# Performance work log

Hardware: AMD Instinct MI355X
Metric: run time of the kernel (lower is better)

The kernel has to match this reference:

```python
import jax, jax.numpy as jnp
import numpy as np
import math

B, NOUT, NCLASSES, CENTER, TOPK = 1024, 512, 5994, 3, 5
M, SUB_M, SCALE = 0.2, -0.06, 30.0

COS_M, SIN_M = math.cos(M), math.sin(M)
TH, MM = math.cos(math.pi - M), math.sin(math.pi - M) * M
SUB_COS_M, SUB_SIN_M = math.cos(SUB_M), math.sin(SUB_M)
SUB_TH, SUB_MM = math.cos(math.pi - SUB_M), math.sin(math.pi - SUB_M) * SUB_M


def setup_inputs() -> dict:
    key = jax.random.key(0)
    k1, k2, k3 = jax.random.split(key, 3)
    x = jax.random.normal(k1, (B, NOUT), dtype=jnp.float32)
    # xavier_normal over (center, nClasses, nOut): fan_in=nClasses*nOut, fan_out=center*nOut
    std = math.sqrt(2.0 / (NCLASSES * NOUT + CENTER * NOUT))
    weight = jax.random.normal(k2, (CENTER, NCLASSES, NOUT), dtype=jnp.float32) * std
    label = jax.random.randint(k3, (B,), 0, NCLASSES, dtype=jnp.int64)
    return {"x": x, "weight": weight, "label": label}


def _l2norm(v, axis=-1, eps=1e-12):
    return v / jnp.maximum(jnp.linalg.norm(v, axis=axis, keepdims=True), eps)


def reference(x, weight, label):
    xn = _l2norm(x)                       # [B, j]
    wn = _l2norm(weight)                  # [a, c, j]
    cosine_subcen = jnp.einsum('bj,acj->bac', xn, wn)   # [B, center, C]
    cosine = jnp.max(cosine_subcen, axis=1)             # [B, C]

    sine = jnp.sqrt(jnp.clip(1.0 - cosine * cosine, 0.0, 1.0))
    phi = jnp.where(cosine - TH > 0, cosine * COS_M - sine * SIN_M, cosine - MM)
    sub_phi = jnp.where(cosine - SUB_TH > 0,
                        cosine * SUB_COS_M - sine * SUB_SIN_M,
                        cosine - SUB_MM)

    # topk+1 candidates; drop the label column if present, else drop the last
    _, idx = jax.lax.top_k(cosine, TOPK + 1)            # [B, topk+1]
    is_label = (idx == label[:, None].astype(idx.dtype))
    # stable sort pushes the (unique) label hit to the end, preserving order otherwise
    order = jnp.argsort(is_label.astype(jnp.int32), axis=1, stable=True)
    idx_fixed = jnp.take_along_axis(idx, order[:, :TOPK], axis=1)   # [B, topk]

    rows = jnp.arange(B)[:, None]
    one_hot_sub = jnp.zeros_like(cosine).at[rows, idx_fixed].add(1.0)
    one_hot = jax.nn.one_hot(label, NCLASSES, dtype=cosine.dtype)

    output = (one_hot * phi + one_hot_sub * sub_phi
              + (1.0 - one_hot_sub - one_hot) * cosine) * SCALE

    logp = jax.nn.log_softmax(output, axis=-1)
    loss = -jnp.mean(logp[jnp.arange(B), label])

    pred = jnp.argmax(cosine * SCALE, axis=-1)
    prec1 = jnp.mean((pred == label).astype(jnp.float32)) * 100.0
    return loss, prec1
```

## Files before the change

### kernel.cpp

```cpp
#include <hip/hip_runtime.h>
#include <math.h>

#define NB 1024
#define NC 5994
#define NCP 6144
#define NK 512
#define NA 3
#define NT 48
#define SCALE_F 30.0f
#define NPT 24

#define COS_M_F 0.9800665778412416f
#define SIN_M_F 0.19866933079506122f
#define TH_F (-0.9800665778412416f)
#define MM_F 0.039733866159012244f
#define SUB_COS_M_F 0.9982005399352042f
#define SUB_SIN_M_F (-0.05996400647944459f)
#define SUB_TH_F (-0.9982005399352042f)
#define SUB_MM_F 0.0035978403887666754f

typedef __attribute__((ext_vector_type(8))) short short8;
typedef __attribute__((ext_vector_type(4))) float f32x4;

__device__ __forceinline__ float waveReduceSum(float v) {
#pragma unroll
  for (int off = 32; off > 0; off >>= 1) v += __shfl_down(v, off);
  return v;
}

__device__ __forceinline__ void waveArgMax(float& v, int& i) {
#pragma unroll
  for (int off = 32; off > 0; off >>= 1) {
    float ov = __shfl_down(v, off);
    int oi = __shfl_down(i, off);
    if (ov > v || (ov == v && (unsigned)oi < (unsigned)i)) { v = ov; i = oi; }
  }
}

__device__ __forceinline__ ushort f2bf(float f) {
  unsigned u = __float_as_uint(f);
  u += 0x7FFFu + ((u >> 16) & 1u);
  return (ushort)(u >> 16);
}

__device__ __forceinline__ void load_lds16(const ushort* g, ushort* l) {
  __builtin_amdgcn_global_load_lds(
      (const __attribute__((address_space(1))) unsigned int*)g,
      (__attribute__((address_space(3))) unsigned int*)l, 16, 0, 0);
}

__global__ __launch_bounds__(256) void norm_convert(const float* __restrict__ x,
                                                    const float* __restrict__ w,
                                                    ushort* __restrict__ xb,
                                                    ushort* __restrict__ wb) {
  const int row = blockIdx.x * 4 + (threadIdx.x >> 6);
  const int lane = threadIdx.x & 63;
  const float* src;
  ushort* dst;
  if (row < NB) {
    src = x + (size_t)row * NK;
    dst = xb + (size_t)row * NK;
  } else {
    const int r = row - NB;
    const int a = r / NCP, c = r % NCP;
    dst = wb + (size_t)r * NK;
    if (c >= NC) {
      ushort4 z = {0, 0, 0, 0};
      *(ushort4*)(dst + lane * 4) = z;
      *(ushort4*)(dst + 256 + lane * 4) = z;
      return;
    }
    src = w + ((size_t)a * NC + c) * NK;
  }
  const float4 v0 = *(const float4*)(src + lane * 4);
  const float4 v1 = *(const float4*)(src + 256 + lane * 4);
  float ss = v0.x * v0.x + v0.y * v0.y + v0.z * v0.z + v0.w * v0.w +
             v1.x * v1.x + v1.y * v1.y + v1.z * v1.z + v1.w * v1.w;
  ss = waveReduceSum(ss);
  ss = __shfl(ss, 0);
  const float rn = 1.0f / fmaxf(sqrtf(ss), 1e-12f);
  ushort4 o0 = {f2bf(v0.x * rn), f2bf(v0.y * rn), f2bf(v0.z * rn), f2bf(v0.w * rn)};
  ushort4 o1 = {f2bf(v1.x * rn), f2bf(v1.y * rn), f2bf(v1.z * rn), f2bf(v1.w * rn)};
  *(ushort4*)(dst + lane * 4) = o0;
  *(ushort4*)(dst + 256 + lane * 4) = o1;
}

__global__ __launch_bounds__(128) void cos_gemm_mfma(const ushort* __restrict__ Xb,
                                                     const ushort* __restrict__ Wb,
                                                     float* __restrict__ cosine) {
  __shared__ ushort sA0[64 * 32];
  __shared__ ushort sA1[64 * 32];
  __shared__ ushort sB0[128 * 32];
  __shared__ ushort sB1[128 * 32];
  const int tid = threadIdx.x;
  const int lane = tid & 63;
  const int w = tid >> 6;

  const int id = blockIdx.x;
  const int resid = id & 7;
  const int by = (id >> 3) & 15;
  const int chunk = id >> 7;
  const int cx = chunk * 8 + resid;
  const int b0 = by * 64;
  const int c0 = cx * 128;

  const int lrow = lane >> 2;
  const int lcol8 = (lane & 3) * 8;
  const ushort* gA = Xb + (size_t)(b0 + 32 * w + lrow) * NK + lcol8;
  const ushort* gB = Wb + (size_t)(c0 + 64 * w + lrow) * NK + lcol8;
  const int ldsA = w * 1024;
  const int ldsB = w * 2048;

  const int r = lane & 15;
  const int kg = lane >> 4;
  const int offA = r * 32 + kg * 8;
  const int offB = (w * 64 + r) * 32 + kg * 8;

  f32x4 best[4][4];
  f32x4 acc[4][4];
#pragma unroll
  for (int i = 0; i < 4; ++i)
#pragma unroll
    for (int j = 0; j < 4; ++j) {
#pragma unroll
      for (int q = 0; q < 4; ++q) best[i][j][q] = -INFINITY;
      acc[i][j] = (f32x4)(0.f);
    }

  load_lds16(gA, (ushort*)sA0 + ldsA);
  load_lds16(gA + 16 * NK, (ushort*)sA0 + ldsA + 512);
#pragma unroll
  for (int j = 0; j < 4; ++j)
    load_lds16(gB + j * 16 * NK, (ushort*)sB0 + ldsB + j * 512);
  __syncthreads();

#define GEMM_BODY(T, SAr, SBr, SAw, SBw)                                        \
  {                                                                             \
    const int t_ = (T);                                                         \
    if (t_ + 1 < NT) {                                                          \
      const int tn = t_ + 1;                                                    \
      const int k0 = (tn & 15) << 5;                                            \
      const size_t boff = (size_t)(tn >> 4) * NCP * NK;                         \
      load_lds16(gA + k0, (ushort*)SAw + ldsA);                                 \
      load_lds16(gA + k0 + 16 * NK, (ushort*)SAw + ldsA + 512);                 \
      _Pragma("unroll") for (int j = 0; j < 4; ++j)                             \
          load_lds16(gB + boff + k0 + j * 16 * NK,                              \
                     (ushort*)SBw + ldsB + j * 512);                            \
    }                                                                           \
    short8 af[4], bf[4];                                                        \
    _Pragma("unroll") for (int mi = 0; mi < 4; ++mi)                            \
        af[mi] = *(const short8*)&SAr[offA + mi * 512];                         \
    _Pragma("unroll") for (int ni = 0; ni < 4; ++ni)                            \
        bf[ni] = *(const short8*)&SBr[offB + ni * 512];                         \
    _Pragma("unroll") for (int mi = 0; mi < 4; ++mi)                            \
        _Pragma("unroll") for (int ni = 0; ni < 4; ++ni)                        \
            acc[mi][ni] = __builtin_amdgcn_mfma_f32_16x16x32_bf16(              \
                af[mi], bf[ni], acc[mi][ni], 0, 0, 0);                          \
    if ((t_ & 15) == 15) {                                                      \
      _Pragma("unroll") for (int i = 0; i < 4; ++i)                             \
          _Pragma("unroll") for (int j = 0; j < 4; ++j) {                       \
        _Pragma("unroll") for (int q = 0; q < 4; ++q)                           \
            best[i][j][q] = fmaxf(best[i][j][q], acc[i][j][q]);                 \
        acc[i][j] = (f32x4)(0.f);                                               \
      }                                                                         \
    }                                                                           \
    __syncthreads();                                                            \
  }

  for (int t = 0; t < NT; t += 2) {
    GEMM_BODY(t, sA0, sB0, sA1, sB1)
    GEMM_BODY(t + 1, sA1, sB1, sA0, sB0)
  }
#undef GEMM_BODY

  const int q4 = (lane >> 4) * 4;
#pragma unroll
  for (int ni = 0; ni < 4; ++ni) {
    const int col = c0 + w * 64 + ni * 16 + r;
    if (col < NC) {
#pragma unroll
      for (int mi = 0; mi < 4; ++mi) {
        const int row0 = b0 + mi * 16 + q4;
#pragma unroll
        for (int q = 0; q < 4; ++q)
          cosine[(size_t)(row0 + q) * NC + col] = best[mi][ni][q];
      }
    }
  }
}

__global__ __launch_bounds__(256) void row_loss(const float* __restrict__ cosine,
                                                const int* __restrict__ label,
                                                float* __restrict__ loss_b,
                                                float* __restrict__ corr_b) {
  __shared__ float swv[4];
  __shared__ int swi[4];
  __shared__ float s_red[4];
  __shared__ float s_maxv;
  __shared__ float s_cosL;
  __shared__ float topv[6];
  __shared__ int topi[6];

  const int b = blockIdx.x, tid = threadIdx.x;
  const int wv = tid >> 6;
  const int lab = label[b];
  const float* row = cosine + (size_t)b * NC;

  float v[NPT];
  float bv = -INFINITY;
  int bi = -1;
#pragma unroll
  for (int j = 0; j < NPT; ++j) {
    const int i = tid + j * 256;
    v[j] = (i < NC) ? row[i] : -INFINITY;
    if (v[j] > bv) { bv = v[j]; bi = i; }
  }
  if (tid == (lab & 255)) s_cosL = v[lab >> 8];
  waveArgMax(bv, bi);
  if ((tid & 63) == 0) { swv[wv] = bv; swi[wv] = bi; }
  __syncthreads();
  if (tid == 0) {
    float mv = swv[0]; int mi = swi[0];
    for (int q = 1; q < 4; ++q)
      if (swv[q] > mv || (swv[q] == mv && (unsigned)swi[q] < (unsigned)mi)) { mv = swv[q]; mi = swi[q]; }
    s_maxv = mv; topv[0] = mv; topi[0] = mi;
  }
  __syncthreads();
  const float maxv = s_maxv;

  float ps = 0.f;
#pragma unroll
  for (int j = 0; j < NPT; ++j) ps += __expf(SCALE_F * (v[j] - maxv));
  ps = waveReduceSum(ps);
  if ((tid & 63) == 0) s_red[wv] = ps;

  unsigned excl = 0;
  {
    const int wi = topi[0];
    if ((wi & 255) == tid) excl |= 1u << (wi >> 8);
  }

  for (int e = 1; e < 6; ++e) {
    float lv = -INFINITY;
    int li = -1;
#pragma unroll
    for (int j = 0; j < NPT; ++j)
      if (!((excl >> j) & 1u) && v[j] > lv) { lv = v[j]; li = tid + j * 256; }
    waveArgMax(lv, li);
    if ((tid & 63) == 0) { swv[wv] = lv; swi[wv] = li; }
    __syncthreads();
    if (tid == 0) {
      float mv = swv[0]; int mi = swi[0];
      for (int q = 1; q < 4; ++q)
        if (swv[q] > mv || (swv[q] == mv && (unsigned)swi[q] < (unsigned)mi)) { mv = swv[q]; mi = swi[q]; }
      topv[e] = mv; topi[e] = mi;
    }
    __syncthreads();
    const int wi = topi[e];
    if ((wi & 255) == tid) excl |= 1u << (wi >> 8);
  }

  if (tid == 0) {
    const float S = s_red[0] + s_red[1] + s_red[2] + s_red[3];
    const float m = SCALE_F * maxv;
    const float cosL = s_cosL;
    const float sineL = sqrtf(fminf(fmaxf(1.f - cosL * cosL, 0.f), 1.f));
    const float phiL = (cosL - TH_F > 0.f) ? (cosL * COS_M_F - sineL * SIN_M_F) : (cosL - MM_F);
    float adj = __expf(SCALE_F * phiL - m) - __expf(SCALE_F * cosL - m);
    int cnt = 0;
    for (int e = 0; e < 6 && cnt < 5; ++e) {
      if (topi[e] == lab) continue;
      const float c = topv[e];
      const float sine = sqrtf(fminf(fmaxf(1.f - c * c, 0.f), 1.f));
      const float sp = (c - SUB_TH_F > 0.f) ? (c * SUB_COS_M_F - sine * SUB_SIN_M_F) : (c - SUB_MM_F);
      adj += __expf(SCALE_F * sp - m) - __expf(SCALE_F * c - m);
      ++cnt;
    }
    const float Sp = S + adj;
    loss_b[b] = (logf(Sp) + m) - SCALE_F * phiL;
    corr_b[b] = (topi[0] == lab) ? 1.f : 0.f;
  }
}

__global__ __launch_bounds__(256) void finalize(const float* __restrict__ loss_b,
                                                const float* __restrict__ corr_b,
                                                float* __restrict__ out) {
  const int tid = threadIdx.x;
  float ls = 0.f, cs = 0.f;
  for (int i = tid; i < NB; i += 256) { ls += loss_b[i]; cs += corr_b[i]; }
  ls = waveReduceSum(ls);
  cs = waveReduceSum(cs);
  __shared__ float sl[4], sc[4];
  if ((tid & 63) == 0) { sl[tid >> 6] = ls; sc[tid >> 6] = cs; }
  __syncthreads();
  if (tid == 0) {
    const float L = sl[0] + sl[1] + sl[2] + sl[3];
    const float Cr = sc[0] + sc[1] + sc[2] + sc[3];
    out[0] = L / (float)NB;
    out[1] = Cr / (float)NB * 100.f;
  }
}

extern "C" void kernel_launch(void* const* d_in, const int* in_sizes, int n_in,
                              void* d_out, int out_size, void* d_ws, size_t ws_size,
                              hipStream_t stream) {
  const float* x = (const float*)d_in[0];
  const float* w = (const float*)d_in[1];
  const int* label = (const int*)d_in[2];
  float* out = (float*)d_out;
  char* ws = (char*)d_ws;

  ushort* xb = (ushort*)ws;
  ushort* wb = (ushort*)(ws + 1048576);
  float* cosine = (float*)(ws + 1048576 + 18874368);
  float* loss_b = (float*)ws;
  float* corr_b = (float*)(ws + 4096);

  norm_convert<<<(NB + NA * NCP) / 4, 256, 0, stream>>>(x, w, xb, wb);
  cos_gemm_mfma<<<16 * 48, 128, 0, stream>>>(xb, wb, cosine);
  row_loss<<<NB, 256, 0, stream>>>(cosine, label, loss_b, corr_b);
  finalize<<<1, 256, 0, stream>>>(loss_b, corr_b, out);
}
```

Measured before the change: 68.10 us.

## Assign one wavefront per row in loss kernel and relayout GEMM LDS tiles

The row-loss kernel now gives each 64-lane wavefront a whole row, held in 94 registers per lane. Top-k and the row max are done with wave shuffles only, which removes the block-level __syncthreads and shared-memory reductions across 4 waves. The top-5 entries are masked out of the register array and their exp terms added back separately. The GEMM loader now writes tiles into LDS in the MFMA fragment order (row r, k-group kg), so fragment reads become lane*8 contiguous. Holding a full row per lane raises register pressure and may cut occupancy or cause spills, and the fully unrolled masking loops add instructions.

Result: slower. 99.71 us (+46.4%).

```diff
diff --git a/kernel.cpp b/kernel.cpp
--- a/kernel.cpp
+++ b/kernel.cpp
@@ -8,7 +8,7 @@
 #define NA 3
 #define NT 48
 #define SCALE_F 30.0f
-#define NPT 24
+#define NV 94
 
 #define COS_M_F 0.9800665778412416f
 #define SIN_M_F 0.19866933079506122f
@@ -97,24 +97,19 @@
   const int w = tid >> 6;
 
   const int id = blockIdx.x;
-  const int resid = id & 7;
+  const int cx = (id & 7) + ((id >> 7) << 3);
   const int by = (id >> 3) & 15;
-  const int chunk = id >> 7;
-  const int cx = chunk * 8 + resid;
   const int b0 = by * 64;
   const int c0 = cx * 128;
 
-  const int lrow = lane >> 2;
-  const int lcol8 = (lane & 3) * 8;
-  const ushort* gA = Xb + (size_t)(b0 + 32 * w + lrow) * NK + lcol8;
-  const ushort* gB = Wb + (size_t)(c0 + 64 * w + lrow) * NK + lcol8;
+  const int r = lane & 15;
+  const int kg = lane >> 4;
+  const int l8 = lane * 8;
+  const ushort* gA = Xb + (size_t)(b0 + w * 32 + r) * NK + kg * 8;
+  const ushort* gB = Wb + (size_t)(c0 + w * 64 + r) * NK + kg * 8;
   const int ldsA = w * 1024;
   const int ldsB = w * 2048;
-
-  const int r = lane & 15;
-  const int kg = lane >> 4;
-  const int offA = r * 32 + kg * 8;
-  const int offB = (w * 64 + r) * 32 + kg * 8;
+  const int w4 = w * 4;
 
   f32x4 best[4][4];
   f32x4 acc[4][4];
@@ -131,7 +126,7 @@
   load_lds16(gA + 16 * NK, (ushort*)sA0 + ldsA + 512);
 #pragma unroll
   for (int j = 0; j < 4; ++j)
-    load_lds16(gB + j * 16 * NK, (ushort*)sB0 + ldsB + j * 512);
+    load_lds16(gB + (size_t)j * 16 * NK, (ushort*)sB0 + ldsB + j * 512);
   __syncthreads();
 
 #define GEMM_BODY(T, SAr, SBr, SAw, SBw)                                        \
@@ -140,18 +135,18 @@
     if (t_ + 1 < NT) {                                                          \
       const int tn = t_ + 1;                                                    \
       const int k0 = (tn & 15) << 5;                                            \
-      const size_t boff = (size_t)(tn >> 4) * NCP * NK;                         \
+      const size_t boff = (size_t)(tn >> 4) * NCP * NK + k0;                    \
       load_lds16(gA + k0, (ushort*)SAw + ldsA);                                 \
       load_lds16(gA + k0 + 16 * NK, (ushort*)SAw + ldsA + 512);                 \
       _Pragma("unroll") for (int j = 0; j < 4; ++j)                             \
-          load_lds16(gB + boff + k0 + j * 16 * NK,                              \
+          load_lds16(gB + boff + (size_t)j * 16 * NK,                           \
                      (ushort*)SBw + ldsB + j * 512);                            \
     }                                                                           \
     short8 af[4], bf[4];                                                        \
     _Pragma("unroll") for (int mi = 0; mi < 4; ++mi)                            \
-        af[mi] = *(const short8*)&SAr[offA + mi * 512];                         \
+        af[mi] = *(const short8*)&SAr[mi * 512 + l8];                           \
     _Pragma("unroll") for (int ni = 0; ni < 4; ++ni)                            \
-        bf[ni] = *(const short8*)&SBr[offB + ni * 512];                         \
+        bf[ni] = *(const short8*)&SBr[(w4 + ni) * 512 + l8];                    \
     _Pragma("unroll") for (int mi = 0; mi < 4; ++mi)                            \
         _Pragma("unroll") for (int ni = 0; ni < 4; ++ni)                        \
             acc[mi][ni] = __builtin_amdgcn_mfma_f32_16x16x32_bf16(              \
@@ -193,83 +188,64 @@
                                                 const int* __restrict__ label,
                                                 float* __restrict__ loss_b,
                                                 float* __restrict__ corr_b) {
-  __shared__ float swv[4];
-  __shared__ int swi[4];
-  __shared__ float s_red[4];
-  __shared__ float s_maxv;
-  __shared__ float s_cosL;
-  __shared__ float topv[6];
-  __shared__ int topi[6];
-
-  const int b = blockIdx.x, tid = threadIdx.x;
-  const int wv = tid >> 6;
-  const int lab = label[b];
-  const float* row = cosine + (size_t)b * NC;
-
-  float v[NPT];
-  float bv = -INFINITY;
-  int bi = -1;
-#pragma unroll
-  for (int j = 0; j < NPT; ++j) {
-    const int i = tid + j * 256;
-    v[j] = (i < NC) ? row[i] : -INFINITY;
-    if (v[j] > bv) { bv = v[j]; bi = i; }
-  }
-  if (tid == (lab & 255)) s_cosL = v[lab >> 8];
-  waveArgMax(bv, bi);
-  if ((tid & 63) == 0) { swv[wv] = bv; swi[wv] = bi; }
-  __syncthreads();
-  if (tid == 0) {
-    float mv = swv[0]; int mi = swi[0];
-    for (int q = 1; q < 4; ++q)
-      if (swv[q] > mv || (swv[q] == mv && (unsigned)swi[q] < (unsigned)mi)) { mv = swv[q]; mi = swi[q]; }
-    s_maxv = mv; topv[0] = mv; topi[0] = mi;
-  }
-  __syncthreads();
-  const float maxv = s_maxv;
+  const int row = blockIdx.x * 4 + (threadIdx.x >> 6);
+  const int lane = threadIdx.x & 63;
+  const int lab = label[row];
+  const float* rp = cosine + (size_t)row * NC;
+
+  float v[NV];
+#pragma unroll
+  for (int e = 0; e < NV; ++e) {
+    const int idx = e * 64 + lane;
+    v[e] = (idx < NC) ? rp[idx] : -INFINITY;
+  }
+
+  float cl = -INFINITY;
+#pragma unroll
+  for (int e = 0; e < NV; ++e)
+    if (e * 64 + lane == lab) cl = v[e];
+  const float cosL = __shfl(cl, lab & 63);
+
+  float topv[6];
+  int topi[6];
+#pragma unroll
+  for (int e6 = 0; e6 < 6; ++e6) {
+    float bv = -INFINITY;
+    int bi = 0x7FFFFFFF;
+#pragma unroll
+    for (int e = 0; e < NV; ++e)
+      if (v[e] > bv) { bv = v[e]; bi = e * 64 + lane; }
+    waveArgMax(bv, bi);
+    bv = __shfl(bv, 0);
+    bi = __shfl(bi, 0);
+    topv[e6] = bv;
+    topi[e6] = bi;
+    if (e6 < 5 && (bi & 63) == lane) {
+      const int ke = bi >> 6;
+#pragma unroll
+      for (int e = 0; e < NV; ++e)
+        if (e == ke) v[e] = -INFINITY;
+    }
+  }
+  const float maxv = topv[0];
 
   float ps = 0.f;
 #pragma unroll
-  for (int j = 0; j < NPT; ++j) ps += __expf(SCALE_F * (v[j] - maxv));
+  for (int e = 0; e < NV; ++e) ps += __expf(SCALE_F * (v[e] - maxv));
   ps = waveReduceSum(ps);
-  if ((tid & 63) == 0) s_red[wv] = ps;
-
-  unsigned excl = 0;
-  {
-    const int wi = topi[0];
-    if ((wi & 255) == tid) excl |= 1u << (wi >> 8);
-  }
-
-  for (int e = 1; e < 6; ++e) {
-    float lv = -INFINITY;
-    int li = -1;
-#pragma unroll
-    for (int j = 0; j < NPT; ++j)
-      if (!((excl >> j) & 1u) && v[j] > lv) { lv = v[j]; li = tid + j * 256; }
-    waveArgMax(lv, li);
-    if ((tid & 63) == 0) { swv[wv] = lv; swi[wv] = li; }
-    __syncthreads();
-    if (tid == 0) {
-      float mv = swv[0]; int mi = swi[0];
-      for (int q = 1; q < 4; ++q)
-        if (swv[q] > mv || (swv[q] == mv && (unsigned)swi[q] < (unsigned)mi)) { mv = swv[q]; mi = swi[q]; }
-      topv[e] = mv; topi[e] = mi;
-    }
-    __syncthreads();
-    const int wi = topi[e];
-    if ((wi & 255) == tid) excl |= 1u << (wi >> 8);
-  }
-
-  if (tid == 0) {
-    const float S = s_red[0] + s_red[1] + s_red[2] + s_red[3];
+
+  if (lane == 0) {
+    float S = ps;
+#pragma unroll
+    for (int e6 = 0; e6 < 5; ++e6) S += __expf(SCALE_F * (topv[e6] - maxv));
     const float m = SCALE_F * maxv;
-    const float cosL = s_cosL;
     const float sineL = sqrtf(fminf(fmaxf(1.f - cosL * cosL, 0.f), 1.f));
     const float phiL = (cosL - TH_F > 0.f) ? (cosL * COS_M_F - sineL * SIN_M_F) : (cosL - MM_F);
     float adj = __expf(SCALE_F * phiL - m) - __expf(SCALE_F * cosL - m);
     int cnt = 0;
-    for (int e = 0; e < 6 && cnt < 5; ++e) {
-      if (topi[e] == lab) continue;
+#pragma unroll
+    for (int e = 0; e < 6; ++e) {
+      if (topi[e] == lab || cnt >= 5) continue;
       const float c = topv[e];
       const float sine = sqrtf(fminf(fmaxf(1.f - c * c, 0.f), 1.f));
       const float sp = (c - SUB_TH_F > 0.f) ? (c * SUB_COS_M_F - sine * SUB_SIN_M_F) : (c - SUB_MM_F);
@@ -277,8 +253,8 @@
       ++cnt;
     }
     const float Sp = S + adj;
-    loss_b[b] = (logf(Sp) + m) - SCALE_F * phiL;
-    corr_b[b] = (topi[0] == lab) ? 1.f : 0.f;
+    loss_b[row] = (logf(Sp) + m) - SCALE_F * phiL;
+    corr_b[row] = (topi[0] == lab) ? 1.f : 0.f;
   }
 }
 
@@ -318,6 +294,6 @@
 
   norm_convert<<<(NB + NA * NCP) / 4, 256, 0, stream>>>(x, w, xb, wb);
   cos_gemm_mfma<<<16 * 48, 128, 0, stream>>>(xb, wb, cosine);
-  row_loss<<<NB, 256, 0, stream>>>(cosine, label, loss_b, corr_b);
+  row_loss<<<NB / 4, 256, 0, stream>>>(cosine, label, loss_b, corr_b);
   finalize<<<1, 256, 0, stream>>>(loss_b, corr_b, out);
 }
```
